# Kernel optimization log

Hardware: AMD Instinct MI355X
Metric: run time of the kernel (lower is better)

Reference implementation:

```python
import jax, jax.numpy as jnp
import numpy as np

B, T, D, H = 32, 512, 1024, 1024  # batch, seq, input_size, hidden_size


def _xavier(key, shape):
    fan_in, fan_out = shape
    limit = float(np.sqrt(6.0 / (fan_in + fan_out)))
    return jax.random.uniform(key, shape, jnp.float32, -limit, limit)


def setup_inputs() -> dict:
    key = jax.random.key(0)
    k1, k2, k3 = jax.random.split(key, 3)
    x = jax.random.normal(k1, (B, T, D), jnp.float32)
    weight_ih = _xavier(k2, (D, 4 * H))
    weight_hh = _xavier(k3, (H, 4 * H))
    bias = jnp.zeros((4 * H,), jnp.float32)
    return {"x": x, "weight_ih": weight_ih, "weight_hh": weight_hh, "bias": bias}


def _lstm(x, weight_ih, weight_hh, bias):
    HS = weight_hh.shape[0]
    bs = x.shape[0]
    # Precompute input projections for all timesteps in one big GEMM.
    x_proj = jnp.einsum('btd,dg->btg', x, weight_ih) + bias  # [B,T,4H]
    h0 = jnp.zeros((bs, HS), x.dtype)
    c0 = jnp.zeros((bs, HS), x.dtype)

    def step(carry, xp_t):
        h, c = carry
        gates = xp_t + h @ weight_hh  # [B,4H]
        i_t = jax.nn.sigmoid(gates[:, :HS])
        f_t = jax.nn.sigmoid(gates[:, HS:2 * HS])
        g_t = jnp.tanh(gates[:, 2 * HS:3 * HS])
        o_t = jax.nn.sigmoid(gates[:, 3 * HS:])
        c = f_t * c + i_t * g_t
        h = o_t * jnp.tanh(c)
        return (h, c), h

    (h_T, c_T), hs = jax.lax.scan(step, (h0, c0), jnp.swapaxes(x_proj, 0, 1))
    hidden_seq = jnp.swapaxes(hs, 0, 1)  # [B,T,H]
    return hidden_seq, (h_T, c_T)


def reference(x, weight_ih, weight_hh, bias):
    return _lstm(x, weight_ih, weight_hh, bias)
```

## Files before the change

### kernel.cpp

```cpp
#include <hip/hip_runtime.h>

typedef unsigned short ushort_t;
typedef unsigned int   uint32;
typedef unsigned long long ull_t;
typedef __attribute__((ext_vector_type(8))) short short8;
typedef __attribute__((ext_vector_type(4))) float floatx4;

#define B_    32
#define T_    512
#define H_    1024
#define G4_   4096
#define HSEQ_ (B_*T_*H_)

#define NBLK 64

#define XPROJ_OFF 0ul
#define WTIH_OFF  134217728ul
#define WTHH_OFF  142606336ul
#define H0X_OFF   150994944ul
#define H1X_OFF   151060480ul
#define FLAGS_OFF 151126016ul
#define WS_NEED   151130112ul

#define H0_OFF  0ul
#define H1_OFF  65536ul
#define CTR_OFF 131072ul

__device__ __forceinline__ ushort_t f2b_rne(float f) {
    uint32 u = __float_as_uint(f);
    u += 0x7fffu + ((u >> 16) & 1u);
    return (ushort_t)(u >> 16);
}
__device__ __forceinline__ float b2f(ushort_t u) { return __uint_as_float(((uint32)u) << 16); }
__device__ __forceinline__ float sigm(float x)  { return 1.f / (1.f + __expf(-x)); }
__device__ __forceinline__ float tanh_(float x) { return 1.f - 2.f / (__expf(2.f * x) + 1.f); }

__global__ void transpose_cvt(const float* __restrict__ in, ushort_t* __restrict__ out)
{
    const int id = blockIdx.x * 256 + threadIdx.x;
    const int n  = id & 4095;
    const int k0 = (id >> 12) * 8;
    union { ushort_t v[8]; uint4 q; } r;
#pragma unroll
    for (int j = 0; j < 8; j++)
        r.v[j] = f2b_rne(in[(size_t)(k0 + j) * G4_ + n]);
    *(uint4*)(out + (size_t)n * 1024 + k0) = r.q;
}

__launch_bounds__(256, 2)
__global__ void gemm_xproj(const float* __restrict__ A, const ushort_t* __restrict__ Bt,
                           const float* __restrict__ bias, ushort_t* __restrict__ C)
{
    __shared__ ushort_t As[128 * 32];
    __shared__ ushort_t Bs[128 * 32];
    const int tid = threadIdx.x;
    const int wave = tid >> 6, lane = tid & 63, l16 = lane & 15, quad = lane >> 4;
    const int wm = (wave >> 1) * 64, wn = (wave & 1) * 64;
    const int m0 = blockIdx.y * 128, n0 = blockIdx.x * 128;
    const int r = tid >> 2;
    const int kp = (tid & 3) * 8;

    floatx4 acc[4][4];
#pragma unroll
    for (int i = 0; i < 4; i++)
#pragma unroll
        for (int j = 0; j < 4; j++) acc[i][j] = (floatx4){0.f, 0.f, 0.f, 0.f};

    for (int kk = 0; kk < 1024; kk += 32) {
#pragma unroll
        for (int h = 0; h < 2; h++) {
            const float* ap = A + (size_t)(m0 + r + h * 64) * 1024 + kk + kp;
            const uint4 u0 = *(const uint4*)ap;
            const uint4 u1 = *(const uint4*)(ap + 4);
            uint4 p;
            p.x = __builtin_amdgcn_perm(u0.y, u0.x, 0x07060302u);
            p.y = __builtin_amdgcn_perm(u0.w, u0.z, 0x07060302u);
            p.z = __builtin_amdgcn_perm(u1.y, u1.x, 0x07060302u);
            p.w = __builtin_amdgcn_perm(u1.w, u1.z, 0x07060302u);
            *(uint4*)&As[(r + h * 64) * 32 + kp] = p;
        }
        const ushort_t* bp = Bt + (size_t)(n0 + r) * 1024 + kk + kp;
        *(uint4*)&Bs[r * 32 + kp]        = *(const uint4*)bp;
        *(uint4*)&Bs[(r + 64) * 32 + kp] = *(const uint4*)(bp + 64 * 1024);
        __syncthreads();

        short8 af[4], bfr[4];
#pragma unroll
        for (int i = 0; i < 4; i++) af[i]  = *(const short8*)&As[(wm + i * 16 + l16) * 32 + quad * 8];
#pragma unroll
        for (int j = 0; j < 4; j++) bfr[j] = *(const short8*)&Bs[(wn + j * 16 + l16) * 32 + quad * 8];
#pragma unroll
        for (int i = 0; i < 4; i++)
#pragma unroll
            for (int j = 0; j < 4; j++)
                acc[i][j] = __builtin_amdgcn_mfma_f32_16x16x32_bf16(af[i], bfr[j], acc[i][j], 0, 0, 0);
        __syncthreads();
    }

#pragma unroll
    for (int i = 0; i < 4; i++) {
        const int gm = m0 + wm + i * 16 + quad * 4;
#pragma unroll
        for (int j = 0; j < 4; j++) {
            const int gn = n0 + wn + j * 16 + l16;
            const float bv = bias[gn];
#pragma unroll
            for (int rr = 0; rr < 4; rr++)
                C[(size_t)(gm + rr) * G4_ + gn] = f2b_rne(acc[i][j][rr] + bv);
        }
    }
}

__launch_bounds__(512, 2)
__global__ void lstm_scan_xp(const ushort_t* __restrict__ xproj,
                             const ushort_t* __restrict__ wthh,
                             ushort_t* __restrict__ h0buf,
                             ushort_t* __restrict__ h1buf,
                             float* __restrict__ out,
                             uint32* __restrict__ flags)
{
    const int tid  = threadIdx.x;
    const int bid  = blockIdx.x;
    const int wave = tid >> 6, lane = tid & 63, l16 = lane & 15, quad = lane >> 4;
    const int g     = wave & 3;
    const int khalf = wave >> 2;
    const int unit0 = bid * 16;
    const int col0  = g * 1024 + unit0 + l16;

    __shared__ ushort_t hs[32 * 1024];
    __shared__ float gA[4 * 32 * 17];
    __shared__ float gB[4 * 32 * 17];

    short8 whf[16];
#pragma unroll
    for (int kk = 0; kk < 16; kk++)
        whf[kk] = *(const short8*)(wthh + (size_t)col0 * 1024 + khalf * 512 + kk * 32 + quad * 8);

    const int eb = tid >> 4, ej = tid & 15;
    const int hwoff = (bid >> 1) * 1024 + eb * 32 + 16 * (bid & 1) + ej;
    float cst = 0.f;

    const int b0 = l16, b1 = l16 + 16;
    const int off0 = (b0 * 64 + quad * 16) ^ ((b0 & 7) << 4);
    const int off1 = (b1 * 64 + quad * 16) ^ ((b1 & 7) << 4);
    const int rowbase = khalf * 16 * 2048;

    const int src0  = wave * 8;
    const int abase = (lane >> 1) * 64 + (lane & 1) * 16;

    ushort_t xq[4];
    {
        const ushort_t* xp = xproj + ((size_t)eb * T_ + 0) * G4_ + unit0 + ej;
#pragma unroll
        for (int gg = 0; gg < 4; gg++) xq[gg] = xp[gg * 1024];
    }

    for (int t = 0; t < 512; t++) {
        const ushort_t* hr = (t & 1) ? h1buf : h0buf;
        ushort_t*       hw = (t & 1) ? h0buf : h1buf;

        for (;;) {
            int rdy = 1;
            if (lane < 8)
                rdy = (__hip_atomic_load(&flags[(src0 + lane) * 16],
                                         __ATOMIC_RELAXED, __HIP_MEMORY_SCOPE_AGENT)
                       >= (uint32)t);
            if (__ballot(rdy) == ~0ull) break;
        }

        {
            ull_t d0[8], d1[8];
#pragma unroll
            for (int sl = 0; sl < 8; sl++) {
                const int S = src0 + sl;
                const size_t a = (size_t)(S >> 1) * 2048 + (size_t)((S & 1) * 32 + abase);
                const char* p = (const char*)hr + a;
                d0[sl] = __hip_atomic_load((const ull_t*)p,
                                           __ATOMIC_RELAXED, __HIP_MEMORY_SCOPE_AGENT);
                d1[sl] = __hip_atomic_load((const ull_t*)(p + 8),
                                           __ATOMIC_RELAXED, __HIP_MEMORY_SCOPE_AGENT);
            }
#pragma unroll
            for (int sl = 0; sl < 8; sl++) {
                const int S = src0 + sl;
                const int c = ((S >> 1) * 2048 + (S & 1) * 32 + abase) >> 4;
                const int dst = (c * 16) ^ (((c >> 2) & 7) << 4);
                uint4 v;
                *(ull_t*)&v.x = d0[sl];
                *(ull_t*)&v.z = d1[sl];
                *(uint4*)((char*)hs + dst) = v;
            }
        }
        __syncthreads();

        floatx4 a0a = (floatx4){0.f, 0.f, 0.f, 0.f};
        floatx4 a0b = a0a, a1a = a0a, a1b = a0a;
#pragma unroll
        for (int kk = 0; kk < 16; kk++) {
            const char* base = (const char*)hs + rowbase + kk * 2048;
            const short8 a0 = *(const short8*)(base + off0);
            const short8 a1 = *(const short8*)(base + off1);
            if (kk & 1) {
                a0b = __builtin_amdgcn_mfma_f32_16x16x32_bf16(a0, whf[kk], a0b, 0, 0, 0);
                a1b = __builtin_amdgcn_mfma_f32_16x16x32_bf16(a1, whf[kk], a1b, 0, 0, 0);
            } else {
                a0a = __builtin_amdgcn_mfma_f32_16x16x32_bf16(a0, whf[kk], a0a, 0, 0, 0);
                a1a = __builtin_amdgcn_mfma_f32_16x16x32_bf16(a1, whf[kk], a1a, 0, 0, 0);
            }
        }
        const floatx4 s0 = a0a + a0b;
        const floatx4 s1 = a1a + a1b;
        float* gd = khalf ? gB : gA;
#pragma unroll
        for (int rr = 0; rr < 4; rr++) {
            gd[(g * 32 + quad * 4 + rr) * 17 + l16]      = s0[rr];
            gd[(g * 32 + 16 + quad * 4 + rr) * 17 + l16] = s1[rr];
        }
        __syncthreads();

        float hval, cval;
        {
            const float gi = gA[(0 * 32 + eb) * 17 + ej] + gB[(0 * 32 + eb) * 17 + ej] + b2f(xq[0]);
            const float gf = gA[(1 * 32 + eb) * 17 + ej] + gB[(1 * 32 + eb) * 17 + ej] + b2f(xq[1]);
            const float gg = gA[(2 * 32 + eb) * 17 + ej] + gB[(2 * 32 + eb) * 17 + ej] + b2f(xq[2]);
            const float go = gA[(3 * 32 + eb) * 17 + ej] + gB[(3 * 32 + eb) * 17 + ej] + b2f(xq[3]);
            const float iv = sigm(gi);
            const float fv = sigm(gf);
            const float gv = tanh_(gg);
            const float ov = sigm(go);
            cval = fv * cst + iv * gv;
            cst = cval;
            hval = ov * tanh_(cval);
        }

        {
            const uint32 myb = (uint32)f2b_rne(hval);
            const uint32 nbb = (uint32)__shfl_xor((int)myb, 1);
            if ((ej & 1) == 0)
                __hip_atomic_store((uint32*)(hw + hwoff), myb | (nbb << 16),
                                   __ATOMIC_RELAXED, __HIP_MEMORY_SCOPE_AGENT);
        }

        if (t < 511) {
            __syncthreads();
            if (tid == 0)
                __hip_atomic_store(&flags[bid * 16], (uint32)(t + 1),
                                   __ATOMIC_RELAXED, __HIP_MEMORY_SCOPE_AGENT);
            out[((size_t)eb * T_ + t) * H_ + unit0 + ej] = hval;
            {
                const ushort_t* xp = xproj + ((size_t)eb * T_ + (t + 1)) * G4_ + unit0 + ej;
#pragma unroll
                for (int gg = 0; gg < 4; gg++) xq[gg] = xp[gg * 1024];
            }
        } else {
            out[((size_t)eb * T_ + t) * H_ + unit0 + ej] = hval;
            out[HSEQ_ + eb * H_ + unit0 + ej] = hval;
            out[HSEQ_ + B_ * H_ + eb * H_ + unit0 + ej] = cval;
        }
    }
}

__launch_bounds__(512, 2)
__global__ void lstm_scan_fused(const float* __restrict__ x,
                                const float* __restrict__ wih,
                                const float* __restrict__ whh,
                                const float* __restrict__ bias,
                                ushort_t* __restrict__ h0buf,
                                ushort_t* __restrict__ h1buf,
                                float* __restrict__ out,
                                uint32* __restrict__ ctr)
{
    const int tid  = threadIdx.x;
    const int bid  = blockIdx.x;
    const int wave = tid >> 6, lane = tid & 63, l16 = lane & 15, quad = lane >> 4;
    const int g     = wave & 3;
    const int khalf = wave >> 2;
    const int unit0 = bid * 16;
    const int col0  = g * 1024 + unit0 + l16;
    const int kbase = khalf * 512;

    __shared__ ushort_t xs[32 * 1024];
    __shared__ float gA[4 * 32 * 17];
    __shared__ float gB[4 * 32 * 17];

    short8 wif[16], whf[16];
#pragma unroll
    for (int kk = 0; kk < 16; kk++) {
        short8 vi, vh;
#pragma unroll
        for (int j = 0; j < 8; j++) {
            const size_t k = (size_t)(kbase + kk * 32 + quad * 8 + j);
            vi[j] = (short)f2b_rne(wih[k * G4_ + col0]);
            vh[j] = (short)f2b_rne(whh[k * G4_ + col0]);
        }
        wif[kk] = vi;
        whf[kk] = vh;
    }
    const float bcol = (khalf == 0) ? bias[col0] : 0.f;

    const int eb = tid >> 4, ej = tid & 15;
    const int hwoff = (bid >> 1) * 1024 + eb * 32 + 16 * (bid & 1) + ej;
    float cst = 0.f;

    floatx4 a0a, a0b, a1a, a1b;

    {
        const int sb = tid >> 4, sc = tid & 15;
        const float* xrow = x + ((size_t)sb * T_ + 0) * H_ + sc * 64;
#pragma unroll
        for (int q = 0; q < 8; q++) {
            const uint4 u0 = *(const uint4*)(xrow + q * 8);
            const uint4 u1 = *(const uint4*)(xrow + q * 8 + 4);
            uint4 p;
            p.x = __builtin_amdgcn_perm(u0.y, u0.x, 0x07060302u);
            p.y = __builtin_amdgcn_perm(u0.w, u0.z, 0x07060302u);
            p.z = __builtin_amdgcn_perm(u1.y, u1.x, 0x07060302u);
            p.w = __builtin_amdgcn_perm(u1.w, u1.z, 0x07060302u);
            const int k = sc * 64 + q * 8;
            *(uint4*)&xs[(k >> 5) * 1024 + sb * 32 + (k & 31)] = p;
        }
    }
    __syncthreads();
    a0a = (floatx4){bcol, bcol, bcol, bcol};
    a1a = a0a;
    a0b = (floatx4){0.f, 0.f, 0.f, 0.f};
    a1b = a0b;
#pragma unroll
    for (int kk = 0; kk < 16; kk++) {
        const ushort_t* ps = &xs[(khalf * 16 + kk) * 1024 + quad * 8];
        const short8 a0 = *(const short8*)(ps + l16 * 32);
        const short8 a1 = *(const short8*)(ps + (16 + l16) * 32);
        if (kk & 1) {
            a0b = __builtin_amdgcn_mfma_f32_16x16x32_bf16(a0, wif[kk], a0b, 0, 0, 0);
            a1b = __builtin_amdgcn_mfma_f32_16x16x32_bf16(a1, wif[kk], a1b, 0, 0, 0);
        } else {
            a0a = __builtin_amdgcn_mfma_f32_16x16x32_bf16(a0, wif[kk], a0a, 0, 0, 0);
            a1a = __builtin_amdgcn_mfma_f32_16x16x32_bf16(a1, wif[kk], a1a, 0, 0, 0);
        }
    }

    for (int t = 0; t < 512; t++) {
        const ushort_t* hr = (t & 1) ? h1buf : h0buf;
        ushort_t*       hw = (t & 1) ? h0buf : h1buf;

#pragma unroll
        for (int kk = 0; kk < 16; kk++) {
            const ushort_t* pa = hr + (khalf * 16 + kk) * 1024 + quad * 8;
            const short8 a0 = *(const short8*)(pa + l16 * 32);
            const short8 a1 = *(const short8*)(pa + (16 + l16) * 32);
            if (kk & 1) {
                a0b = __builtin_amdgcn_mfma_f32_16x16x32_bf16(a0, whf[kk], a0b, 0, 0, 0);
                a1b = __builtin_amdgcn_mfma_f32_16x16x32_bf16(a1, whf[kk], a1b, 0, 0, 0);
            } else {
                a0a = __builtin_amdgcn_mfma_f32_16x16x32_bf16(a0, whf[kk], a0a, 0, 0, 0);
                a1a = __builtin_amdgcn_mfma_f32_16x16x32_bf16(a1, whf[kk], a1a, 0, 0, 0);
            }
        }
        const floatx4 s0 = a0a + a0b;
        const floatx4 s1 = a1a + a1b;
        float* gd = khalf ? gB : gA;
#pragma unroll
        for (int rr = 0; rr < 4; rr++) {
            gd[(g * 32 + quad * 4 + rr) * 17 + l16]      = s0[rr];
            gd[(g * 32 + 16 + quad * 4 + rr) * 17 + l16] = s1[rr];
        }
        __syncthreads();

        {
            const float gi = gA[(0 * 32 + eb) * 17 + ej] + gB[(0 * 32 + eb) * 17 + ej];
            const float gf = gA[(1 * 32 + eb) * 17 + ej] + gB[(1 * 32 + eb) * 17 + ej];
            const float gg = gA[(2 * 32 + eb) * 17 + ej] + gB[(2 * 32 + eb) * 17 + ej];
            const float go = gA[(3 * 32 + eb) * 17 + ej] + gB[(3 * 32 + eb) * 17 + ej];
            const float iv = sigm(gi);
            const float fv = sigm(gf);
            const float gv = tanh_(gg);
            const float ov = sigm(go);
            const float c = fv * cst + iv * gv;
            cst = c;
            const float h = ov * tanh_(c);
            hw[hwoff] = f2b_rne(h);
            out[((size_t)eb * T_ + t) * H_ + unit0 + ej] = h;
            if (t == 511) {
                out[HSEQ_ + eb * H_ + unit0 + ej] = h;
                out[HSEQ_ + B_ * H_ + eb * H_ + unit0 + ej] = cst;
            }
        }
        __syncthreads();

        if (t < 511) {
            if (tid == 0) {
                __threadfence();
                __hip_atomic_fetch_add(ctr, 1u, __ATOMIC_RELAXED, __HIP_MEMORY_SCOPE_AGENT);
            }
            {
                const int sb = tid >> 4, sc = tid & 15;
                const float* xrow = x + ((size_t)sb * T_ + (t + 1)) * H_ + sc * 64;
#pragma unroll
                for (int q = 0; q < 8; q++) {
                    const uint4 u0 = *(const uint4*)(xrow + q * 8);
                    const uint4 u1 = *(const uint4*)(xrow + q * 8 + 4);
                    uint4 p;
                    p.x = __builtin_amdgcn_perm(u0.y, u0.x, 0x07060302u);
                    p.y = __builtin_amdgcn_perm(u0.w, u0.z, 0x07060302u);
                    p.z = __builtin_amdgcn_perm(u1.y, u1.x, 0x07060302u);
                    p.w = __builtin_amdgcn_perm(u1.w, u1.z, 0x07060302u);
                    const int k = sc * 64 + q * 8;
                    *(uint4*)&xs[(k >> 5) * 1024 + sb * 32 + (k & 31)] = p;
                }
            }
            __syncthreads();
            a0a = (floatx4){bcol, bcol, bcol, bcol};
            a1a = a0a;
            a0b = (floatx4){0.f, 0.f, 0.f, 0.f};
            a1b = a0b;
#pragma unroll
            for (int kk = 0; kk < 16; kk++) {
                const ushort_t* ps = &xs[(khalf * 16 + kk) * 1024 + quad * 8];
                const short8 a0 = *(const short8*)(ps + l16 * 32);
                const short8 a1 = *(const short8*)(ps + (16 + l16) * 32);
                if (kk & 1) {
                    a0b = __builtin_amdgcn_mfma_f32_16x16x32_bf16(a0, wif[kk], a0b, 0, 0, 0);
                    a1b = __builtin_amdgcn_mfma_f32_16x16x32_bf16(a1, wif[kk], a1b, 0, 0, 0);
                } else {
                    a0a = __builtin_amdgcn_mfma_f32_16x16x32_bf16(a0, wif[kk], a0a, 0, 0, 0);
                    a1a = __builtin_amdgcn_mfma_f32_16x16x32_bf16(a1, wif[kk], a1a, 0, 0, 0);
                }
            }
            if (tid == 0) {
                const uint32 target = (uint32)NBLK * (uint32)(t + 1);
                while (__hip_atomic_load(ctr, __ATOMIC_RELAXED, __HIP_MEMORY_SCOPE_AGENT) < target) {
                    __builtin_amdgcn_s_sleep(1);
                }
                __threadfence();
            }
            __syncthreads();
        }
    }
}

extern "C" void kernel_launch(void* const* d_in, const int* in_sizes, int n_in,
                              void* d_out, int out_size, void* d_ws, size_t ws_size,
                              hipStream_t stream)
{
    const float* x    = (const float*)d_in[0];
    const float* wih  = (const float*)d_in[1];
    const float* whh  = (const float*)d_in[2];
    const float* bias = (const float*)d_in[3];
    float* out = (float*)d_out;
    char* ws = (char*)d_ws;

    if (ws_size >= WS_NEED) {
        ushort_t* xproj = (ushort_t*)(ws + XPROJ_OFF);
        ushort_t* wtih  = (ushort_t*)(ws + WTIH_OFF);
        ushort_t* wthh  = (ushort_t*)(ws + WTHH_OFF);
        ushort_t* h0    = (ushort_t*)(ws + H0X_OFF);
        ushort_t* h1    = (ushort_t*)(ws + H1X_OFF);
        uint32*   flags = (uint32*)(ws + FLAGS_OFF);

        hipMemsetAsync(ws + H0X_OFF, 0, 2 * 65536 + 4096, stream);
        hipLaunchKernelGGL(transpose_cvt, dim3(2048), dim3(256), 0, stream, wih, wtih);
        hipLaunchKernelGGL(transpose_cvt, dim3(2048), dim3(256), 0, stream, whh, wthh);
        hipLaunchKernelGGL(gemm_xproj, dim3(32, 128), dim3(256), 0, stream,
                           x, wtih, bias, xproj);
        hipLaunchKernelGGL(lstm_scan_xp, dim3(NBLK), dim3(512), 0, stream,
                           xproj, wthh, h0, h1, out, flags);
    } else {
        ushort_t* h0  = (ushort_t*)(ws + H0_OFF);
        ushort_t* h1  = (ushort_t*)(ws + H1_OFF);
        uint32*   ctr = (uint32*)(ws + CTR_OFF);

        hipMemsetAsync(ws, 0, 131072 + 256, stream);
        hipLaunchKernelGGL(lstm_scan_fused, dim3(NBLK), dim3(512), 0, stream,
                           x, wih, whh, bias, h0, h1, out, ctr);
    }
}
```

Before: 2.458 ms.

## Split recurrent GEMM by batch halves, fuse gate activations, replace barrier with counter

Result: slower. 2.651 ms (+7.9%).

```diff
diff --git a/kernel.cpp b/kernel.cpp
--- a/kernel.cpp
+++ b/kernel.cpp
@@ -111,7 +111,7 @@
     }
 }
 
-__launch_bounds__(512, 2)
+__launch_bounds__(512, 1)
 __global__ void lstm_scan_xp(const ushort_t* __restrict__ xproj,
                              const ushort_t* __restrict__ wthh,
                              ushort_t* __restrict__ h0buf,
@@ -123,37 +123,38 @@
     const int bid  = blockIdx.x;
     const int wave = tid >> 6, lane = tid & 63, l16 = lane & 15, quad = lane >> 4;
     const int g     = wave & 3;
-    const int khalf = wave >> 2;
+    const int bh    = wave >> 2;
     const int unit0 = bid * 16;
     const int col0  = g * 1024 + unit0 + l16;
 
     __shared__ ushort_t hs[32 * 1024];
-    __shared__ float gA[4 * 32 * 17];
-    __shared__ float gB[4 * 32 * 17];
-
-    short8 whf[16];
-#pragma unroll
-    for (int kk = 0; kk < 16; kk++)
-        whf[kk] = *(const short8*)(wthh + (size_t)col0 * 1024 + khalf * 512 + kk * 32 + quad * 8);
+    __shared__ float    gL[4 * 32 * 17];
+    __shared__ uint32   cnt;
+
+    short8 whf[32];
+#pragma unroll
+    for (int kk = 0; kk < 32; kk++)
+        whf[kk] = *(const short8*)(wthh + (size_t)col0 * 1024 + kk * 32 + quad * 8);
+
+    if (tid == 0) cnt = 0;
 
     const int eb = tid >> 4, ej = tid & 15;
     const int hwoff = (bid >> 1) * 1024 + eb * 32 + 16 * (bid & 1) + ej;
     float cst = 0.f;
 
-    const int b0 = l16, b1 = l16 + 16;
-    const int off0 = (b0 * 64 + quad * 16) ^ ((b0 & 7) << 4);
-    const int off1 = (b1 * 64 + quad * 16) ^ ((b1 & 7) << 4);
-    const int rowbase = khalf * 16 * 2048;
+    const int brow = bh * 16 + l16;
+    const int off0 = (brow * 64 + quad * 16) ^ ((l16 & 7) << 4);
 
     const int src0  = wave * 8;
     const int abase = (lane >> 1) * 64 + (lane & 1) * 16;
 
+    const size_t xcol = (size_t)g * 1024 + unit0 + l16;
     ushort_t xq[4];
-    {
-        const ushort_t* xp = xproj + ((size_t)eb * T_ + 0) * G4_ + unit0 + ej;
-#pragma unroll
-        for (int gg = 0; gg < 4; gg++) xq[gg] = xp[gg * 1024];
-    }
+#pragma unroll
+    for (int rr = 0; rr < 4; rr++)
+        xq[rr] = xproj[((size_t)(bh * 16 + quad * 4 + rr) * T_ + 0) * G4_ + xcol];
+
+    __syncthreads();
 
     for (int t = 0; t < 512; t++) {
         const ushort_t* hr = (t & 1) ? h1buf : h0buf;
@@ -193,41 +194,36 @@
         }
         __syncthreads();
 
-        floatx4 a0a = (floatx4){0.f, 0.f, 0.f, 0.f};
-        floatx4 a0b = a0a, a1a = a0a, a1b = a0a;
-#pragma unroll
-        for (int kk = 0; kk < 16; kk++) {
-            const char* base = (const char*)hs + rowbase + kk * 2048;
+        floatx4 ac0 = (floatx4){0.f, 0.f, 0.f, 0.f};
+        floatx4 ac1 = ac0, ac2 = ac0, ac3 = ac0;
+#pragma unroll
+        for (int kk = 0; kk < 32; kk += 4) {
+            const char* base = (const char*)hs + kk * 2048;
             const short8 a0 = *(const short8*)(base + off0);
-            const short8 a1 = *(const short8*)(base + off1);
-            if (kk & 1) {
-                a0b = __builtin_amdgcn_mfma_f32_16x16x32_bf16(a0, whf[kk], a0b, 0, 0, 0);
-                a1b = __builtin_amdgcn_mfma_f32_16x16x32_bf16(a1, whf[kk], a1b, 0, 0, 0);
-            } else {
-                a0a = __builtin_amdgcn_mfma_f32_16x16x32_bf16(a0, whf[kk], a0a, 0, 0, 0);
-                a1a = __builtin_amdgcn_mfma_f32_16x16x32_bf16(a1, whf[kk], a1a, 0, 0, 0);
-            }
-        }
-        const floatx4 s0 = a0a + a0b;
-        const floatx4 s1 = a1a + a1b;
-        float* gd = khalf ? gB : gA;
+            const short8 a1 = *(const short8*)(base + 2048 + off0);
+            const short8 a2 = *(const short8*)(base + 4096 + off0);
+            const short8 a3 = *(const short8*)(base + 6144 + off0);
+            ac0 = __builtin_amdgcn_mfma_f32_16x16x32_bf16(a0, whf[kk],     ac0, 0, 0, 0);
+            ac1 = __builtin_amdgcn_mfma_f32_16x16x32_bf16(a1, whf[kk + 1], ac1, 0, 0, 0);
+            ac2 = __builtin_amdgcn_mfma_f32_16x16x32_bf16(a2, whf[kk + 2], ac2, 0, 0, 0);
+            ac3 = __builtin_amdgcn_mfma_f32_16x16x32_bf16(a3, whf[kk + 3], ac3, 0, 0, 0);
+        }
+        floatx4 s = (ac0 + ac1) + (ac2 + ac3);
+
 #pragma unroll
         for (int rr = 0; rr < 4; rr++) {
-            gd[(g * 32 + quad * 4 + rr) * 17 + l16]      = s0[rr];
-            gd[(g * 32 + 16 + quad * 4 + rr) * 17 + l16] = s1[rr];
+            const float v = s[rr] + b2f(xq[rr]);
+            const float a = (g == 2) ? tanh_(v) : sigm(v);
+            gL[(g * 32 + bh * 16 + quad * 4 + rr) * 17 + l16] = a;
         }
         __syncthreads();
 
         float hval, cval;
         {
-            const float gi = gA[(0 * 32 + eb) * 17 + ej] + gB[(0 * 32 + eb) * 17 + ej] + b2f(xq[0]);
-            const float gf = gA[(1 * 32 + eb) * 17 + ej] + gB[(1 * 32 + eb) * 17 + ej] + b2f(xq[1]);
-            const float gg = gA[(2 * 32 + eb) * 17 + ej] + gB[(2 * 32 + eb) * 17 + ej] + b2f(xq[2]);
-            const float go = gA[(3 * 32 + eb) * 17 + ej] + gB[(3 * 32 + eb) * 17 + ej] + b2f(xq[3]);
-            const float iv = sigm(gi);
-            const float fv = sigm(gf);
-            const float gv = tanh_(gg);
-            const float ov = sigm(go);
+            const float iv = gL[(0 * 32 + eb) * 17 + ej];
+            const float fv = gL[(1 * 32 + eb) * 17 + ej];
+            const float gv = gL[(2 * 32 + eb) * 17 + ej];
+            const float ov = gL[(3 * 32 + eb) * 17 + ej];
             cval = fv * cst + iv * gv;
             cst = cval;
             hval = ov * tanh_(cval);
@@ -242,16 +238,18 @@
         }
 
         if (t < 511) {
-            __syncthreads();
-            if (tid == 0)
-                __hip_atomic_store(&flags[bid * 16], (uint32)(t + 1),
-                                   __ATOMIC_RELAXED, __HIP_MEMORY_SCOPE_AGENT);
             out[((size_t)eb * T_ + t) * H_ + unit0 + ej] = hval;
-            {
-                const ushort_t* xp = xproj + ((size_t)eb * T_ + (t + 1)) * G4_ + unit0 + ej;
-#pragma unroll
-                for (int gg = 0; gg < 4; gg++) xq[gg] = xp[gg * 1024];
-            }
+            asm volatile("s_waitcnt vmcnt(0)" ::: "memory");
+            if (lane == 0) {
+                const uint32 old = __hip_atomic_fetch_add(&cnt, 1u,
+                                       __ATOMIC_RELAXED, __HIP_MEMORY_SCOPE_WORKGROUP);
+                if (old == (uint32)(8 * t + 7))
+                    __hip_atomic_store(&flags[bid * 16], (uint32)(t + 1),
+                                       __ATOMIC_RELAXED, __HIP_MEMORY_SCOPE_AGENT);
+            }
+#pragma unroll
+            for (int rr = 0; rr < 4; rr++)
+                xq[rr] = xproj[((size_t)(bh * 16 + quad * 4 + rr) * T_ + (t + 1)) * G4_ + xcol];
         } else {
             out[((size_t)eb * T_ + t) * H_ + unit0 + ej] = hval;
             out[HSEQ_ + eb * H_ + unit0 + ej] = hval;
```

## Replace per-block flag barrier with timestep-tagged hidden-state words

Applied to the files above, without the earlier changes.

New measurement: 4.174 ms. 1.7x slower.

```diff
diff --git a/kernel.cpp b/kernel.cpp
--- a/kernel.cpp
+++ b/kernel.cpp
@@ -17,9 +17,8 @@
 #define XPROJ_OFF 0ul
 #define WTIH_OFF  134217728ul
 #define WTHH_OFF  142606336ul
-#define H0X_OFF   150994944ul
-#define H1X_OFF   151060480ul
-#define FLAGS_OFF 151126016ul
+#define H0T_OFF   WTIH_OFF
+#define H1T_OFF   (WTIH_OFF + 131072ul)
 #define WS_NEED   151130112ul
 
 #define H0_OFF  0ul
@@ -114,10 +113,9 @@
 __launch_bounds__(512, 2)
 __global__ void lstm_scan_xp(const ushort_t* __restrict__ xproj,
                              const ushort_t* __restrict__ wthh,
-                             ushort_t* __restrict__ h0buf,
-                             ushort_t* __restrict__ h1buf,
-                             float* __restrict__ out,
-                             uint32* __restrict__ flags)
+                             ull_t* __restrict__ h0buf,
+                             ull_t* __restrict__ h1buf,
+                             float* __restrict__ out)
 {
     const int tid  = threadIdx.x;
     const int bid  = blockIdx.x;
@@ -137,7 +135,7 @@
         whf[kk] = *(const short8*)(wthh + (size_t)col0 * 1024 + khalf * 512 + kk * 32 + quad * 8);
 
     const int eb = tid >> 4, ej = tid & 15;
-    const int hwoff = (bid >> 1) * 1024 + eb * 32 + 16 * (bid & 1) + ej;
+    const int hw64 = (bid >> 1) * 512 + eb * 16 + (bid & 1) * 8 + (ej >> 1);
     float cst = 0.f;
 
     const int b0 = l16, b1 = l16 + 16;
@@ -146,7 +144,8 @@
     const int rowbase = khalf * 16 * 2048;
 
     const int src0  = wave * 8;
-    const int abase = (lane >> 1) * 64 + (lane & 1) * 16;
+    const int seb   = lane >> 1;
+    const int shalf = lane & 1;
 
     ushort_t xq[4];
     {
@@ -156,40 +155,42 @@
     }
 
     for (int t = 0; t < 512; t++) {
-        const ushort_t* hr = (t & 1) ? h1buf : h0buf;
-        ushort_t*       hw = (t & 1) ? h0buf : h1buf;
-
-        for (;;) {
-            int rdy = 1;
-            if (lane < 8)
-                rdy = (__hip_atomic_load(&flags[(src0 + lane) * 16],
-                                         __ATOMIC_RELAXED, __HIP_MEMORY_SCOPE_AGENT)
-                       >= (uint32)t);
-            if (__ballot(rdy) == ~0ull) break;
-        }
-
+        const ull_t* hr = (t & 1) ? h1buf : h0buf;
+        ull_t*       hw = (t & 1) ? h0buf : h1buf;
+
+        ull_t d[8][4];
         {
-            ull_t d0[8], d1[8];
-#pragma unroll
-            for (int sl = 0; sl < 8; sl++) {
-                const int S = src0 + sl;
-                const size_t a = (size_t)(S >> 1) * 2048 + (size_t)((S & 1) * 32 + abase);
-                const char* p = (const char*)hr + a;
-                d0[sl] = __hip_atomic_load((const ull_t*)p,
-                                           __ATOMIC_RELAXED, __HIP_MEMORY_SCOPE_AGENT);
-                d1[sl] = __hip_atomic_load((const ull_t*)(p + 8),
-                                           __ATOMIC_RELAXED, __HIP_MEMORY_SCOPE_AGENT);
-            }
-#pragma unroll
-            for (int sl = 0; sl < 8; sl++) {
-                const int S = src0 + sl;
-                const int c = ((S >> 1) * 2048 + (S & 1) * 32 + abase) >> 4;
-                const int dst = (c * 16) ^ (((c >> 2) & 7) << 4);
-                uint4 v;
-                *(ull_t*)&v.x = d0[sl];
-                *(ull_t*)&v.z = d1[sl];
-                *(uint4*)((char*)hs + dst) = v;
-            }
+            const uint32 tg = (uint32)t;
+            for (;;) {
+#pragma unroll
+                for (int sl = 0; sl < 8; sl++) {
+                    const int S = src0 + sl;
+                    const ull_t* p = hr + (size_t)((S >> 1) * 512 + seb * 16 + (S & 1) * 8 + shalf * 4);
+#pragma unroll
+                    for (int q = 0; q < 4; q++)
+                        d[sl][q] = __hip_atomic_load(p + q,
+                                       __ATOMIC_RELAXED, __HIP_MEMORY_SCOPE_AGENT);
+                }
+                uint32 bad = 0;
+#pragma unroll
+                for (int sl = 0; sl < 8; sl++)
+#pragma unroll
+                    for (int q = 0; q < 4; q++)
+                        bad |= (uint32)(d[sl][q] >> 32) ^ tg;
+                if (__ballot(bad == 0) == ~0ull) break;
+            }
+        }
+#pragma unroll
+        for (int sl = 0; sl < 8; sl++) {
+            const int S = src0 + sl;
+            const int c = ((S >> 1) * 2048 + (S & 1) * 32 + seb * 64 + shalf * 16) >> 4;
+            const int dst = (c * 16) ^ (((c >> 2) & 7) << 4);
+            uint4 v;
+            v.x = (uint32)d[sl][0];
+            v.y = (uint32)d[sl][1];
+            v.z = (uint32)d[sl][2];
+            v.w = (uint32)d[sl][3];
+            *(uint4*)((char*)hs + dst) = v;
         }
         __syncthreads();
 
@@ -233,19 +234,17 @@
             hval = ov * tanh_(cval);
         }
 
-        {
-            const uint32 myb = (uint32)f2b_rne(hval);
-            const uint32 nbb = (uint32)__shfl_xor((int)myb, 1);
-            if ((ej & 1) == 0)
-                __hip_atomic_store((uint32*)(hw + hwoff), myb | (nbb << 16),
-                                   __ATOMIC_RELAXED, __HIP_MEMORY_SCOPE_AGENT);
-        }
-
         if (t < 511) {
-            __syncthreads();
-            if (tid == 0)
-                __hip_atomic_store(&flags[bid * 16], (uint32)(t + 1),
-                                   __ATOMIC_RELAXED, __HIP_MEMORY_SCOPE_AGENT);
+            {
+                const uint32 myb = (uint32)f2b_rne(hval);
+                const uint32 nbb = (uint32)__shfl_xor((int)myb, 1);
+                if ((ej & 1) == 0) {
+                    const ull_t pk = (ull_t)(myb | (nbb << 16))
+                                   | ((ull_t)(uint32)(t + 1) << 32);
+                    __hip_atomic_store(hw + hw64, pk,
+                                       __ATOMIC_RELAXED, __HIP_MEMORY_SCOPE_AGENT);
+                }
+            }
             out[((size_t)eb * T_ + t) * H_ + unit0 + ej] = hval;
             {
                 const ushort_t* xp = xproj + ((size_t)eb * T_ + (t + 1)) * G4_ + unit0 + ej;
@@ -453,17 +452,16 @@
         ushort_t* xproj = (ushort_t*)(ws + XPROJ_OFF);
         ushort_t* wtih  = (ushort_t*)(ws + WTIH_OFF);
         ushort_t* wthh  = (ushort_t*)(ws + WTHH_OFF);
-        ushort_t* h0    = (ushort_t*)(ws + H0X_OFF);
-        ushort_t* h1    = (ushort_t*)(ws + H1X_OFF);
-        uint32*   flags = (uint32*)(ws + FLAGS_OFF);
-
-        hipMemsetAsync(ws + H0X_OFF, 0, 2 * 65536 + 4096, stream);
+        ull_t*    h0    = (ull_t*)(ws + H0T_OFF);
+        ull_t*    h1    = (ull_t*)(ws + H1T_OFF);
+
         hipLaunchKernelGGL(transpose_cvt, dim3(2048), dim3(256), 0, stream, wih, wtih);
         hipLaunchKernelGGL(transpose_cvt, dim3(2048), dim3(256), 0, stream, whh, wthh);
         hipLaunchKernelGGL(gemm_xproj, dim3(32, 128), dim3(256), 0, stream,
                            x, wtih, bias, xproj);
+        hipMemsetAsync(ws + H0T_OFF, 0, 262144, stream);
         hipLaunchKernelGGL(lstm_scan_xp, dim3(NBLK), dim3(512), 0, stream,
-                           xproj, wthh, h0, h1, out, flags);
+                           xproj, wthh, h0, h1, out);
     } else {
         ushort_t* h0  = (ushort_t*)(ws + H0_OFF);
         ushort_t* h1  = (ushort_t*)(ws + H1_OFF);
```

## Use per-wave flags and split LDS barrier to cut recurrent step sync

Applied to the files above, without the earlier changes.

Result: slower. 2.525 ms (+2.8%).

```diff
diff --git a/kernel.cpp b/kernel.cpp
--- a/kernel.cpp
+++ b/kernel.cpp
@@ -19,7 +19,7 @@
 #define WTHH_OFF  142606336ul
 #define H0X_OFF   150994944ul
 #define H1X_OFF   151060480ul
-#define FLAGS_OFF 151126016ul
+#define FLAGS8_OFF WTIH_OFF
 #define WS_NEED   151130112ul
 
 #define H0_OFF  0ul
@@ -117,7 +117,7 @@
                              ushort_t* __restrict__ h0buf,
                              ushort_t* __restrict__ h1buf,
                              float* __restrict__ out,
-                             uint32* __restrict__ flags)
+                             uint32* __restrict__ flags8)
 {
     const int tid  = threadIdx.x;
     const int bid  = blockIdx.x;
@@ -128,13 +128,15 @@
     const int col0  = g * 1024 + unit0 + l16;
 
     __shared__ ushort_t hs[32 * 1024];
-    __shared__ float gA[4 * 32 * 17];
-    __shared__ float gB[4 * 32 * 17];
+    __shared__ float    gbuf[2][2][4 * 32 * 17];
+    __shared__ uint32   hctr[2];
 
     short8 whf[16];
 #pragma unroll
     for (int kk = 0; kk < 16; kk++)
         whf[kk] = *(const short8*)(wthh + (size_t)col0 * 1024 + khalf * 512 + kk * 32 + quad * 8);
+
+    if (tid == 0) { hctr[0] = 0; hctr[1] = 0; }
 
     const int eb = tid >> 4, ej = tid & 15;
     const int hwoff = (bid >> 1) * 1024 + eb * 32 + 16 * (bid & 1) + ej;
@@ -155,17 +157,18 @@
         for (int gg = 0; gg < 4; gg++) xq[gg] = xp[gg * 1024];
     }
 
+    __syncthreads();
+
     for (int t = 0; t < 512; t++) {
         const ushort_t* hr = (t & 1) ? h1buf : h0buf;
         ushort_t*       hw = (t & 1) ? h0buf : h1buf;
 
-        for (;;) {
-            int rdy = 1;
-            if (lane < 8)
-                rdy = (__hip_atomic_load(&flags[(src0 + lane) * 16],
-                                         __ATOMIC_RELAXED, __HIP_MEMORY_SCOPE_AGENT)
-                       >= (uint32)t);
-            if (__ballot(rdy) == ~0ull) break;
+        {
+            const uint32* fp = flags8 + (size_t)(src0 * 8 + lane) * 16;
+            uint32 v;
+            do {
+                v = __hip_atomic_load(fp, __ATOMIC_RELAXED, __HIP_MEMORY_SCOPE_AGENT);
+            } while (__ballot(v >= (uint32)t) != ~0ull);
         }
 
         {
@@ -191,7 +194,13 @@
                 *(uint4*)((char*)hs + dst) = v;
             }
         }
-        __syncthreads();
+
+        if (lane == 0)
+            __hip_atomic_fetch_add(&hctr[khalf], 1u,
+                                   __ATOMIC_RELEASE, __HIP_MEMORY_SCOPE_WORKGROUP);
+        while (__hip_atomic_load(&hctr[khalf],
+                                 __ATOMIC_ACQUIRE, __HIP_MEMORY_SCOPE_WORKGROUP)
+               < 4u * (uint32)(t + 1)) {}
 
         floatx4 a0a = (floatx4){0.f, 0.f, 0.f, 0.f};
         floatx4 a0b = a0a, a1a = a0a, a1b = a0a;
@@ -210,7 +219,8 @@
         }
         const floatx4 s0 = a0a + a0b;
         const floatx4 s1 = a1a + a1b;
-        float* gd = khalf ? gB : gA;
+
+        float* gd = &gbuf[t & 1][khalf][0];
 #pragma unroll
         for (int rr = 0; rr < 4; rr++) {
             gd[(g * 32 + quad * 4 + rr) * 17 + l16]      = s0[rr];
@@ -218,12 +228,14 @@
         }
         __syncthreads();
 
+        const float* gA_ = &gbuf[t & 1][0][0];
+        const float* gB_ = &gbuf[t & 1][1][0];
         float hval, cval;
         {
-            const float gi = gA[(0 * 32 + eb) * 17 + ej] + gB[(0 * 32 + eb) * 17 + ej] + b2f(xq[0]);
-            const float gf = gA[(1 * 32 + eb) * 17 + ej] + gB[(1 * 32 + eb) * 17 + ej] + b2f(xq[1]);
-            const float gg = gA[(2 * 32 + eb) * 17 + ej] + gB[(2 * 32 + eb) * 17 + ej] + b2f(xq[2]);
-            const float go = gA[(3 * 32 + eb) * 17 + ej] + gB[(3 * 32 + eb) * 17 + ej] + b2f(xq[3]);
+            const float gi = gA_[(0 * 32 + eb) * 17 + ej] + gB_[(0 * 32 + eb) * 17 + ej] + b2f(xq[0]);
+            const float gf = gA_[(1 * 32 + eb) * 17 + ej] + gB_[(1 * 32 + eb) * 17 + ej] + b2f(xq[1]);
+            const float gg = gA_[(2 * 32 + eb) * 17 + ej] + gB_[(2 * 32 + eb) * 17 + ej] + b2f(xq[2]);
+            const float go = gA_[(3 * 32 + eb) * 17 + ej] + gB_[(3 * 32 + eb) * 17 + ej] + b2f(xq[3]);
             const float iv = sigm(gi);
             const float fv = sigm(gf);
             const float gv = tanh_(gg);
@@ -233,18 +245,18 @@
             hval = ov * tanh_(cval);
         }
 
-        {
-            const uint32 myb = (uint32)f2b_rne(hval);
-            const uint32 nbb = (uint32)__shfl_xor((int)myb, 1);
-            if ((ej & 1) == 0)
-                __hip_atomic_store((uint32*)(hw + hwoff), myb | (nbb << 16),
-                                   __ATOMIC_RELAXED, __HIP_MEMORY_SCOPE_AGENT);
-        }
-
         if (t < 511) {
-            __syncthreads();
-            if (tid == 0)
-                __hip_atomic_store(&flags[bid * 16], (uint32)(t + 1),
+            {
+                const uint32 myb = (uint32)f2b_rne(hval);
+                const uint32 nbb = (uint32)__shfl_xor((int)myb, 1);
+                if ((ej & 1) == 0)
+                    __hip_atomic_store((uint32*)(hw + hwoff), myb | (nbb << 16),
+                                       __ATOMIC_RELAXED, __HIP_MEMORY_SCOPE_AGENT);
+            }
+            asm volatile("s_waitcnt vmcnt(0)" ::: "memory");
+            if (lane == 0)
+                __hip_atomic_store(&flags8[(size_t)(bid * 8 + wave) * 16],
+                                   (uint32)(t + 1),
                                    __ATOMIC_RELAXED, __HIP_MEMORY_SCOPE_AGENT);
             out[((size_t)eb * T_ + t) * H_ + unit0 + ej] = hval;
             {
@@ -450,20 +462,21 @@
     char* ws = (char*)d_ws;
 
     if (ws_size >= WS_NEED) {
-        ushort_t* xproj = (ushort_t*)(ws + XPROJ_OFF);
-        ushort_t* wtih  = (ushort_t*)(ws + WTIH_OFF);
-        ushort_t* wthh  = (ushort_t*)(ws + WTHH_OFF);
-        ushort_t* h0    = (ushort_t*)(ws + H0X_OFF);
-        ushort_t* h1    = (ushort_t*)(ws + H1X_OFF);
-        uint32*   flags = (uint32*)(ws + FLAGS_OFF);
-
-        hipMemsetAsync(ws + H0X_OFF, 0, 2 * 65536 + 4096, stream);
+        ushort_t* xproj  = (ushort_t*)(ws + XPROJ_OFF);
+        ushort_t* wtih   = (ushort_t*)(ws + WTIH_OFF);
+        ushort_t* wthh   = (ushort_t*)(ws + WTHH_OFF);
+        ushort_t* h0     = (ushort_t*)(ws + H0X_OFF);
+        ushort_t* h1     = (ushort_t*)(ws + H1X_OFF);
+        uint32*   flags8 = (uint32*)(ws + FLAGS8_OFF);
+
+        hipMemsetAsync(ws + H0X_OFF, 0, 2 * 65536, stream);
         hipLaunchKernelGGL(transpose_cvt, dim3(2048), dim3(256), 0, stream, wih, wtih);
         hipLaunchKernelGGL(transpose_cvt, dim3(2048), dim3(256), 0, stream, whh, wthh);
         hipLaunchKernelGGL(gemm_xproj, dim3(32, 128), dim3(256), 0, stream,
                            x, wtih, bias, xproj);
+        hipMemsetAsync(ws + FLAGS8_OFF, 0, 32768, stream);
         hipLaunchKernelGGL(lstm_scan_xp, dim3(NBLK), dim3(512), 0, stream,
-                           xproj, wthh, h0, h1, out, flags);
+                           xproj, wthh, h0, h1, out, flags8);
     } else {
         ushort_t* h0  = (ushort_t*)(ws + H0_OFF);
         ushort_t* h1  = (ushort_t*)(ws + H1_OFF);
```
